# Optimization experiments

Measured on AMD Instinct MI355X. Metric: run time of the kernel, lower is better.

Reference implementation:

```python
import jax, jax.numpy as jnp
import numpy as np
from math import log2

B, N, H, DH, BSZ = 4, 4096, 16, 64, 16
DIM = H * DH
EPS = 1e-8


def setup_inputs() -> dict:
    key = jax.random.key(0)
    ks = jax.random.split(key, 7)
    s = 0.02
    return {
        "hidden_states": jax.random.normal(ks[0], (B, N, DIM), jnp.float32),
        "Wq": jax.random.normal(ks[1], (DIM, DIM), jnp.float32) * s,
        "bq": jax.random.normal(ks[2], (DIM,), jnp.float32) * s,
        "Wk": jax.random.normal(ks[3], (DIM, DIM), jnp.float32) * s,
        "bk": jax.random.normal(ks[4], (DIM,), jnp.float32) * s,
        "Wv": jax.random.normal(ks[5], (DIM, DIM), jnp.float32) * s,
        "bv": jax.random.normal(ks[6], (DIM,), jnp.float32) * s,
    }


def _hattention(q, k, v):
    # q, k, v: [(b*h), n, dh]; n is a power of two divisible by BSZ
    bh, n, dh = q.shape
    num_levels = int(log2(n // BSZ)) - 2  # coarsen until 4 blocks remain

    # coarsening: mean-pool q and k, sum-pool v (mask=None path)
    qkvs = [(q, k, v)]
    for _ in range(num_levels):
        q = q.reshape(bh, -1, 2, dh).mean(axis=2)
        k = k.reshape(bh, -1, 2, dh).mean(axis=2)
        v = v.reshape(bh, -1, 2, dh).sum(axis=2)
        qkvs.append((q, k, v))

    def flip_blocks(t):
        # swap adjacent blocks to capture off-diagonal interactions
        nb = t.shape[1]
        return t.reshape(bh, nb // 2, 2, BSZ, dh)[:, :, ::-1].reshape(bh, nb, BSZ, dh)

    Ys = []
    L = len(qkvs)
    for ind in range(L):
        qq, kk, vv = qkvs[L - 1 - ind]  # reversed: coarsest first
        is_last = ind == L - 1          # finest level: pure block-diagonal
        blk = lambda t: t.reshape(bh, -1, BSZ, dh)
        qq, kk, vv = blk(qq), blk(kk), blk(vv)
        if not is_last:
            kk = flip_blocks(kk)
            vv = flip_blocks(vv)
        S = jnp.einsum('bnid,bnjd->bnij', qq, kk)
        S = S - jnp.max(S, axis=-1, keepdims=True)
        A = jnp.exp(S)  # unnormalized attention weights
        y = jnp.einsum('bnij,bnjd->bnid', A, vv)
        Ys.append((y.reshape(bh, -1, dh), A.sum(axis=-1).reshape(bh, -1)))

    # interpolate: upsample coarse numerators/denominators and accumulate
    Y, A = Ys[0]
    for Y_l, A_l in Ys[1:]:
        Y = jnp.repeat(Y, 2, axis=1) + Y_l
        A = jnp.repeat(A, 2, axis=1) + A_l
    return Y / (A + EPS)[..., None]


def reference(hidden_states, Wq, bq, Wk, bk, Wv, bv):
    b, n, d = hidden_states.shape
    q = hidden_states @ Wq + bq
    k = hidden_states @ Wk + bk
    v = hidden_states @ Wv + bv
    split_heads = lambda t: t.reshape(b, n, H, DH).transpose(0, 2, 1, 3).reshape(b * H, n, DH)
    q, k, v = split_heads(q), split_heads(k), split_heads(v)
    q = q * (DH ** -0.5)
    out = _hattention(q, k, v)  # [(b*h), n, dh]
    return out.reshape(b, H, n, DH).transpose(0, 2, 1, 3).reshape(b, n, H * DH)
```

## Files before the change

### kernel.cpp

```cpp
#include <hip/hip_runtime.h>
#include <hip/hip_bf16.h>

typedef unsigned short u16;
typedef unsigned int u32;
typedef __bf16 bf16x8 __attribute__((ext_vector_type(8)));
typedef float f32x4 __attribute__((ext_vector_type(4)));
typedef u16 u16x4 __attribute__((ext_vector_type(4)));
typedef u16 u16x8 __attribute__((ext_vector_type(8)));

#define N_    4096
#define H_    16
#define BH_   64
#define DIM_  1024
#define MTOK  16384

#define RB1 262144
#define RB2 393216
#define RB3 458752
#define RB4 491520
#define RB5 507904
#define RB6 516096

__device__ __forceinline__ float bf2f(u16 u) {
  union { u32 i; float f; } x; x.i = ((u32)u) << 16; return x.f;
}
__device__ __forceinline__ u16 f2bf(float f) {
  union { float f; u32 i; } x; x.f = f;
  u32 r = x.i + 0x7fffu + ((x.i >> 16) & 1u);
  return (u16)(r >> 16);
}

__device__ __forceinline__ void gload_lds16(const u16* g, u16* l) {
  __builtin_amdgcn_global_load_lds(
      (const __attribute__((address_space(1))) void*)g,
      (__attribute__((address_space(3))) void*)l, 16, 0, 0);
}

__global__ __launch_bounds__(256) void k_prep(const float* __restrict__ hid,
                                              u16* __restrict__ hidb,
                                              const float* __restrict__ Wq,
                                              const float* __restrict__ Wk,
                                              const float* __restrict__ Wv,
                                              u16* __restrict__ Wt) {
  __shared__ float tile[32][33];
  const int bx = blockIdx.x;
  if (bx < 16384) {
    int i = bx * 256 + threadIdx.x;
    f32x4 v = reinterpret_cast<const f32x4*>(hid)[i];
    u16x4 o;
    o[0] = f2bf(v[0]); o[1] = f2bf(v[1]); o[2] = f2bf(v[2]); o[3] = f2bf(v[3]);
    reinterpret_cast<u16x4*>(hidb)[i] = o;
  } else {
    const int bid = bx - 16384;
    const int zz = bid >> 10;
    const int rem = bid & 1023;
    const int n0 = (rem & 31) * 32, k0 = (rem >> 5) * 32;
    const float* W = (zz == 0) ? Wq : ((zz == 1) ? Wk : Wv);
    const int tx = threadIdx.x & 31, ty = threadIdx.x >> 5;
    #pragma unroll
    for (int r = ty; r < 32; r += 8)
      tile[r][tx] = W[(size_t)(k0 + r) * DIM_ + n0 + tx];
    __syncthreads();
    u16* o = Wt + (size_t)zz * DIM_ * DIM_;
    #pragma unroll
    for (int r = ty; r < 32; r += 8)
      o[(size_t)(n0 + r) * DIM_ + k0 + tx] = f2bf(tile[tx][r]);
  }
}

__global__ __launch_bounds__(256, 2) void k_qkv_gemm(
    const u16* __restrict__ hid,
    const u16* __restrict__ Wt,
    const float* __restrict__ bq, const float* __restrict__ bk, const float* __restrict__ bv,
    u16* __restrict__ qout, u16* __restrict__ kout, u16* __restrict__ vout) {
  const int m0 = blockIdx.x * 128;
  const int n0 = blockIdx.y * 128;
  __shared__ u16 As[128 * 64];
  __shared__ u16 Bs[3][128 * 64];
  const int t = threadIdx.x;
  const int lane = t & 63, wave = t >> 6;
  const int wm = (wave >> 1) * 64, wn = (wave & 1) * 64;
  f32x4 acc[3][4][4];
  #pragma unroll
  for (int z = 0; z < 3; z++)
    #pragma unroll
    for (int m = 0; m < 4; m++)
      #pragma unroll
      for (int n = 0; n < 4; n++) acc[z][m][n] = (f32x4){0.f, 0.f, 0.f, 0.f};

  const int srow = t >> 3;
  const int sslot = (t & 7) ^ (srow & 7);
  const u16* Ag = hid + ((size_t)m0 + srow) * DIM_ + sslot * 8;
  const u16* Bg = Wt + ((size_t)n0 + srow) * DIM_ + sslot * 8;
  u16* AsT = &As[t * 8];
  const int lr = lane & 15, kg = lane >> 4;

  for (int k0 = 0; k0 < DIM_; k0 += 64) {
    #pragma unroll
    for (int j = 0; j < 4; j++)
      gload_lds16(Ag + k0 + j * (32 * DIM_), AsT + j * 2048);
    #pragma unroll
    for (int z = 0; z < 3; z++)
      #pragma unroll
      for (int j = 0; j < 4; j++)
        gload_lds16(Bg + (size_t)z * DIM_ * DIM_ + k0 + j * (32 * DIM_),
                    &Bs[z][t * 8 + j * 2048]);
    __syncthreads();
    #pragma unroll
    for (int ks = 0; ks < 2; ks++) {
      const int sw = ((ks * 4 + kg) ^ (lr & 7)) * 8;
      bf16x8 af[4];
      #pragma unroll
      for (int m = 0; m < 4; m++)
        af[m] = *reinterpret_cast<const bf16x8*>(&As[(wm + m * 16 + lr) * 64 + sw]);
      #pragma unroll
      for (int z = 0; z < 3; z++) {
        bf16x8 bfr[4];
        #pragma unroll
        for (int n = 0; n < 4; n++)
          bfr[n] = *reinterpret_cast<const bf16x8*>(&Bs[z][(wn + n * 16 + lr) * 64 + sw]);
        __builtin_amdgcn_s_setprio(1);
        #pragma unroll
        for (int m = 0; m < 4; m++)
          #pragma unroll
          for (int n = 0; n < 4; n++)
            acc[z][m][n] =
                __builtin_amdgcn_mfma_f32_16x16x32_bf16(af[m], bfr[n], acc[z][m][n], 0, 0, 0);
        __builtin_amdgcn_s_setprio(0);
      }
    }
    __syncthreads();
  }

  const int rg = lane >> 4;
  const int b = m0 >> 12;
  const int posb = m0 & (N_ - 1);
  const int h = (n0 + wn) >> 6;
  const size_t bh = (size_t)(b * H_ + h);

  #pragma unroll
  for (int z = 0; z < 3; z++) {
    const float* bias = (z == 0) ? bq : ((z == 1) ? bk : bv);
    u16* dst = (z == 0) ? qout : ((z == 1) ? kout : vout);
    const float scale = (z == 0) ? 0.125f : 1.0f;
    const bool isv = (z == 2);
    const float s1 = isv ? 1.f : 0.5f, s2 = isv ? 1.f : 0.25f;
    const float s3 = isv ? 1.f : 0.125f, s4 = isv ? 1.f : 0.0625f;
    const float s5 = isv ? 1.f : 0.03125f, s6 = isv ? 1.f : 0.015625f;
    float c5a[4], c5b[4];
    #pragma unroll
    for (int n = 0; n < 4; n++) { c5a[n] = 0.f; c5b[n] = 0.f; }
    #pragma unroll
    for (int m = 0; m < 4; m++) {
      const int plm = wm + m * 16;
      #pragma unroll
      for (int n = 0; n < 4; n++) {
        const int d = n * 16 + lr;
        const float bias_v = bias[n0 + wn + d];
        float v0 = (acc[z][m][n][0] + bias_v) * scale;
        float v1 = (acc[z][m][n][1] + bias_v) * scale;
        float v2 = (acc[z][m][n][2] + bias_v) * scale;
        float v3 = (acc[z][m][n][3] + bias_v) * scale;
        const int pl = plm + rg * 4;
        size_t r0 = (bh * N_ + posb + pl) * 64 + d;
        dst[r0] = f2bf(v0); dst[r0 + 64] = f2bf(v1);
        dst[r0 + 128] = f2bf(v2); dst[r0 + 192] = f2bf(v3);
        float c1a = v0 + v1, c1b = v2 + v3;
        size_t r1 = ((size_t)RB1 + bh * 2048 + (size_t)((posb + pl) >> 1)) * 64 + d;
        dst[r1] = f2bf(c1a * s1);
        dst[r1 + 64] = f2bf(c1b * s1);
        float c2 = c1a + c1b;
        dst[((size_t)RB2 + bh * 1024 + (size_t)((posb + pl) >> 2)) * 64 + d] = f2bf(c2 * s2);
        float c3 = c2 + __shfl_xor(c2, 16);
        float c4 = c3 + __shfl_xor(c3, 32);
        if ((rg & 1) == 0)
          dst[((size_t)RB3 + bh * 512 + (size_t)(((posb + plm) >> 3) + (rg >> 1))) * 64 + d] =
              f2bf(c3 * s3);
        if (rg == 0)
          dst[((size_t)RB4 + bh * 256 + (size_t)((posb + plm) >> 4)) * 64 + d] = f2bf(c4 * s4);
        if (m < 2) c5a[n] += c4; else c5b[n] += c4;
      }
    }
    if (rg == 0) {
      const int r5 = (posb + wm) >> 5;
      const int r6 = (posb + wm) >> 6;
      #pragma unroll
      for (int n = 0; n < 4; n++) {
        const int d = n * 16 + lr;
        dst[((size_t)RB5 + bh * 128 + (size_t)r5) * 64 + d] = f2bf(c5a[n] * s5);
        dst[((size_t)RB5 + bh * 128 + (size_t)(r5 + 1)) * 64 + d] = f2bf(c5b[n] * s5);
        dst[((size_t)RB6 + bh * 64 + (size_t)r6) * 64 + d] = f2bf((c5a[n] + c5b[n]) * s6);
      }
    }
  }
}

__device__ __forceinline__ void qk_softmax(const u16* __restrict__ qb_, size_t qrow,
                                           const u16* __restrict__ kb_, size_t kvrow,
                                           int lane, f32x4& p, float& asum) {
  const int lr = lane & 15, g = lane >> 4;
  const u16* kp = kb_ + (kvrow + lr) * 64 + g * 8;
  const u16* qp = qb_ + (qrow + lr) * 64 + g * 8;
  bf16x8 ka0 = *reinterpret_cast<const bf16x8*>(kp);
  bf16x8 ka1 = *reinterpret_cast<const bf16x8*>(kp + 32);
  bf16x8 qa0 = *reinterpret_cast<const bf16x8*>(qp);
  bf16x8 qa1 = *reinterpret_cast<const bf16x8*>(qp + 32);
  f32x4 s = (f32x4){0.f, 0.f, 0.f, 0.f};
  s = __builtin_amdgcn_mfma_f32_16x16x32_bf16(ka0, qa0, s, 0, 0, 0);
  s = __builtin_amdgcn_mfma_f32_16x16x32_bf16(ka1, qa1, s, 0, 0, 0);
  float mx = fmaxf(fmaxf(s[0], s[1]), fmaxf(s[2], s[3]));
  mx = fmaxf(mx, __shfl_xor(mx, 16));
  mx = fmaxf(mx, __shfl_xor(mx, 32));
  #pragma unroll
  for (int i = 0; i < 4; i++) p[i] = __expf(s[i] - mx);
  asum = p[0] + p[1] + p[2] + p[3];
  asum += __shfl_xor(asum, 16);
  asum += __shfl_xor(asum, 32);
}

__device__ __forceinline__ bf16x8 prep_pb(const f32x4& p, int lane) {
  const int g = lane >> 4;
  const int src = (lane & 15) + ((g & 1) << 5);
  float tl[4], th[4];
  #pragma unroll
  for (int i = 0; i < 4; i++) {
    tl[i] = __shfl(p[i], src);
    th[i] = __shfl(p[i], src + 16);
  }
  const bool act = (g < 2);
  union { u16 u[8]; bf16x8 b; } cvt;
  #pragma unroll
  for (int i = 0; i < 4; i++) {
    cvt.u[i] = act ? f2bf(tl[i]) : (u16)0;
    cvt.u[4 + i] = act ? f2bf(th[i]) : (u16)0;
  }
  return cvt.b;
}

__device__ __forceinline__ f32x4 pv_chunk(const u16* __restrict__ vb_, size_t kvrow,
                                          int c, int lane, bf16x8 pb) {
  const int lr = lane & 15, g = lane >> 4;
  const u16* vp = vb_ + (kvrow + (size_t)(g & 1) * 8) * 64 + c * 16 + lr;
  union { u16 u[8]; bf16x8 b; } va;
  #pragma unroll
  for (int e = 0; e < 8; e++) va.u[e] = vp[(size_t)e * 64];
  f32x4 y = (f32x4){0.f, 0.f, 0.f, 0.f};
  return __builtin_amdgcn_mfma_f32_16x16x32_bf16(va.b, pb, y, 0, 0, 0);
}

__global__ __launch_bounds__(256) void k_attn_rest(
    const u16* __restrict__ qb, const u16* __restrict__ kb, const u16* __restrict__ vb,
    u16* __restrict__ Yb, float* __restrict__ Ab) {
  const int wid = blockIdx.x * 4 + (threadIdx.x >> 6);
  const int lane = threadIdx.x & 63;
  const int rb = wid * 16;
  int r = rb, lnl = 11;
  while (r >= (64 << lnl)) { r -= (64 << lnl); --lnl; }
  const int posl = r & ((1 << lnl) - 1);
  const size_t qrow = (size_t)RB1 + rb;
  const size_t kvrow = qrow - posl + ((size_t)((((posl >> 4) ^ 1)) & ((1 << (lnl - 4)) - 1)) << 4);

  f32x4 p; float asum;
  qk_softmax(qb, qrow, kb, kvrow, lane, p, asum);
  if (lane < 16) Ab[rb + lane] = asum;
  bf16x8 pb = prep_pb(p, lane);

  const int lr = lane & 15, g = lane >> 4;
  #pragma unroll
  for (int c = 0; c < 4; c++) {
    f32x4 y = pv_chunk(vb, kvrow, c, lane, pb);
    u16x4 o;
    #pragma unroll
    for (int i = 0; i < 4; i++) o[i] = f2bf(y[i]);
    *reinterpret_cast<u16x4*>(Yb + (size_t)(rb + lr) * 64 + c * 16 + g * 4) = o;
  }
}

__global__ __launch_bounds__(256) void k_attn0(
    const u16* __restrict__ qb, const u16* __restrict__ kb, const u16* __restrict__ vb,
    const u16* __restrict__ Yb, const float* __restrict__ Ab, float* __restrict__ out) {
  const int wid = blockIdx.x * 4 + (threadIdx.x >> 6);
  const int lane = threadIdx.x & 63;
  const int rb = wid * 16;
  const int bh = rb >> 12, posb = rb & 4095;
  const size_t qrow = (size_t)rb, kvrow = (size_t)rb;

  f32x4 p; float asum;
  qk_softmax(qb, qrow, kb, kvrow, lane, p, asum);
  bf16x8 pb = prep_pb(p, lane);

  const int lr = lane & 15, g = lane >> 4;
  const int pos = posb + lr;
  float den = asum + 1e-8f;
  int ybase[6];
  #pragma unroll
  for (int l = 1; l <= 6; l++) {
    int st = 262144 - (262144 >> (l - 1));
    int idx = st + (bh << (12 - l)) + (pos >> l);
    den += Ab[idx];
    ybase[l - 1] = idx;
  }
  const float inv = 1.0f / den;

  const int b = bh >> 4, h = bh & 15;
  float* op = out + ((size_t)(b * N_ + pos)) * DIM_ + h * 64;
  #pragma unroll
  for (int c = 0; c < 4; c++) {
    f32x4 y = pv_chunk(vb, kvrow, c, lane, pb);
    #pragma unroll
    for (int l = 0; l < 6; l++) {
      u16x4 cy = *reinterpret_cast<const u16x4*>(Yb + (size_t)ybase[l] * 64 + c * 16 + g * 4);
      #pragma unroll
      for (int i = 0; i < 4; i++) y[i] += bf2f(cy[i]);
    }
    f32x4 w;
    #pragma unroll
    for (int i = 0; i < 4; i++) w[i] = y[i] * inv;
    *reinterpret_cast<f32x4*>(op + c * 16 + g * 4) = w;
  }
}

extern "C" void kernel_launch(void* const* d_in, const int* in_sizes, int n_in,
                              void* d_out, int out_size, void* d_ws, size_t ws_size,
                              hipStream_t stream) {
  const float* hid = (const float*)d_in[0];
  const float* Wq = (const float*)d_in[1];
  const float* bq = (const float*)d_in[2];
  const float* Wk = (const float*)d_in[3];
  const float* bk = (const float*)d_in[4];
  const float* Wv = (const float*)d_in[5];
  const float* bv = (const float*)d_in[6];
  float* out = (float*)d_out;
  char* ws = (char*)d_ws;

  u16* hidb = (u16*)(ws + 0);
  u16* Wt   = (u16*)(ws + 33554432);
  u16* Yb   = (u16*)(ws + 0);
  float* Ab = (float*)(ws + 33030144);
  u16* qb   = (u16*)(ws + 39845888);
  u16* kb   = (u16*)(ws + 106430464);
  u16* vb   = (u16*)(ws + 173015040);

  k_prep<<<19456, 256, 0, stream>>>(hid, hidb, Wq, Wk, Wv, Wt);
  k_qkv_gemm<<<dim3(128, 8, 1), 256, 0, stream>>>(hidb, Wt, bq, bk, bv, qb, kb, vb);
  k_attn_rest<<<4032, 256, 0, stream>>>(qb, kb, vb, Yb, Ab);
  k_attn0<<<4096, 256, 0, stream>>>(qb, kb, vb, Yb, Ab, out);
}
```

Baseline: 212.1 us.

## Double-buffer QKV GEMM shared tiles and split work across eight waves

The fused QKV GEMM now uses 512 threads (8 waves, each computing a 32x64 sub-tile) and double-buffers the A/B shared-memory tiles, so the global-to-LDS loads for the next K step are issued before the MFMAs of the current step. Each wave holds half the accumulators, which cuts register pressure. The level-6 pooled sums now span two waves and are combined through an LDS scratch area after a barrier. Shared memory doubles to 128 KB per block, which lowers how many blocks fit on a CU and makes the launch_bounds(512,2) request unlikely to be met.

```diff
diff --git a/kernel.cpp b/kernel.cpp
--- a/kernel.cpp
+++ b/kernel.cpp
@@ -68,75 +68,82 @@
   }
 }
 
-__global__ __launch_bounds__(256, 2) void k_qkv_gemm(
+__global__ __launch_bounds__(512, 2) void k_qkv_gemm(
     const u16* __restrict__ hid,
     const u16* __restrict__ Wt,
     const float* __restrict__ bq, const float* __restrict__ bk, const float* __restrict__ bv,
     u16* __restrict__ qout, u16* __restrict__ kout, u16* __restrict__ vout) {
   const int m0 = blockIdx.x * 128;
   const int n0 = blockIdx.y * 128;
-  __shared__ u16 As[128 * 64];
-  __shared__ u16 Bs[3][128 * 64];
+  __shared__ u16 As[2][8192];
+  __shared__ u16 Bs[2][3][8192];
   const int t = threadIdx.x;
   const int lane = t & 63, wave = t >> 6;
-  const int wm = (wave >> 1) * 64, wn = (wave & 1) * 64;
-  f32x4 acc[3][4][4];
+  const int wm4 = wave >> 1, wn2 = wave & 1;
+  f32x4 acc[3][2][4];
   #pragma unroll
   for (int z = 0; z < 3; z++)
     #pragma unroll
-    for (int m = 0; m < 4; m++)
-      #pragma unroll
-      for (int n = 0; n < 4; n++) acc[z][m][n] = (f32x4){0.f, 0.f, 0.f, 0.f};
+    for (int mf = 0; mf < 2; mf++)
+      #pragma unroll
+      for (int nf = 0; nf < 4; nf++) acc[z][mf][nf] = (f32x4){0.f, 0.f, 0.f, 0.f};
 
   const int srow = t >> 3;
   const int sslot = (t & 7) ^ (srow & 7);
   const u16* Ag = hid + ((size_t)m0 + srow) * DIM_ + sslot * 8;
   const u16* Bg = Wt + ((size_t)n0 + srow) * DIM_ + sslot * 8;
-  u16* AsT = &As[t * 8];
   const int lr = lane & 15, kg = lane >> 4;
 
-  for (int k0 = 0; k0 < DIM_; k0 += 64) {
-    #pragma unroll
-    for (int j = 0; j < 4; j++)
-      gload_lds16(Ag + k0 + j * (32 * DIM_), AsT + j * 2048);
+  auto stage = [&](int d, int k0) {
+    #pragma unroll
+    for (int j = 0; j < 2; j++)
+      gload_lds16(Ag + k0 + j * (64 * DIM_), &As[d][j * 4096 + t * 8]);
     #pragma unroll
     for (int z = 0; z < 3; z++)
       #pragma unroll
-      for (int j = 0; j < 4; j++)
-        gload_lds16(Bg + (size_t)z * DIM_ * DIM_ + k0 + j * (32 * DIM_),
-                    &Bs[z][t * 8 + j * 2048]);
-    __syncthreads();
+      for (int j = 0; j < 2; j++)
+        gload_lds16(Bg + (size_t)z * DIM_ * DIM_ + k0 + j * (64 * DIM_),
+                    &Bs[d][z][j * 4096 + t * 8]);
+  };
+
+  stage(0, 0);
+  __syncthreads();
+  for (int tau = 0; tau < 16; ++tau) {
+    const int cur = tau & 1;
+    if (tau < 15) stage(cur ^ 1, (tau + 1) * 64);
     #pragma unroll
     for (int ks = 0; ks < 2; ks++) {
       const int sw = ((ks * 4 + kg) ^ (lr & 7)) * 8;
-      bf16x8 af[4];
-      #pragma unroll
-      for (int m = 0; m < 4; m++)
-        af[m] = *reinterpret_cast<const bf16x8*>(&As[(wm + m * 16 + lr) * 64 + sw]);
+      bf16x8 af[2];
+      #pragma unroll
+      for (int mf = 0; mf < 2; mf++)
+        af[mf] = *reinterpret_cast<const bf16x8*>(&As[cur][(wm4 * 32 + mf * 16 + lr) * 64 + sw]);
       #pragma unroll
       for (int z = 0; z < 3; z++) {
         bf16x8 bfr[4];
         #pragma unroll
-        for (int n = 0; n < 4; n++)
-          bfr[n] = *reinterpret_cast<const bf16x8*>(&Bs[z][(wn + n * 16 + lr) * 64 + sw]);
+        for (int nf = 0; nf < 4; nf++)
+          bfr[nf] =
+              *reinterpret_cast<const bf16x8*>(&Bs[cur][z][(wn2 * 64 + nf * 16 + lr) * 64 + sw]);
         __builtin_amdgcn_s_setprio(1);
         #pragma unroll
-        for (int m = 0; m < 4; m++)
+        for (int mf = 0; mf < 2; mf++)
           #pragma unroll
-          for (int n = 0; n < 4; n++)
-            acc[z][m][n] =
-                __builtin_amdgcn_mfma_f32_16x16x32_bf16(af[m], bfr[n], acc[z][m][n], 0, 0, 0);
+          for (int nf = 0; nf < 4; nf++)
+            acc[z][mf][nf] =
+                __builtin_amdgcn_mfma_f32_16x16x32_bf16(af[mf], bfr[nf], acc[z][mf][nf], 0, 0, 0);
         __builtin_amdgcn_s_setprio(0);
       }
     }
     __syncthreads();
   }
 
-  const int rg = lane >> 4;
+  const int rg = kg;
   const int b = m0 >> 12;
   const int posb = m0 & (N_ - 1);
-  const int h = (n0 + wn) >> 6;
+  const int h = (n0 >> 6) + wn2;
   const size_t bh = (size_t)(b * H_ + h);
+  float* scr = (float*)&As[0][0];
 
   #pragma unroll
   for (int z = 0; z < 3; z++) {
@@ -146,21 +153,21 @@
     const bool isv = (z == 2);
     const float s1 = isv ? 1.f : 0.5f, s2 = isv ? 1.f : 0.25f;
     const float s3 = isv ? 1.f : 0.125f, s4 = isv ? 1.f : 0.0625f;
-    const float s5 = isv ? 1.f : 0.03125f, s6 = isv ? 1.f : 0.015625f;
-    float c5a[4], c5b[4];
-    #pragma unroll
-    for (int n = 0; n < 4; n++) { c5a[n] = 0.f; c5b[n] = 0.f; }
-    #pragma unroll
-    for (int m = 0; m < 4; m++) {
-      const int plm = wm + m * 16;
-      #pragma unroll
-      for (int n = 0; n < 4; n++) {
-        const int d = n * 16 + lr;
-        const float bias_v = bias[n0 + wn + d];
-        float v0 = (acc[z][m][n][0] + bias_v) * scale;
-        float v1 = (acc[z][m][n][1] + bias_v) * scale;
-        float v2 = (acc[z][m][n][2] + bias_v) * scale;
-        float v3 = (acc[z][m][n][3] + bias_v) * scale;
+    const float s5 = isv ? 1.f : 0.03125f;
+    float c5[4];
+    #pragma unroll
+    for (int nf = 0; nf < 4; nf++) c5[nf] = 0.f;
+    #pragma unroll
+    for (int mf = 0; mf < 2; mf++) {
+      const int plm = wm4 * 32 + mf * 16;
+      #pragma unroll
+      for (int nf = 0; nf < 4; nf++) {
+        const int d = nf * 16 + lr;
+        const float bias_v = bias[n0 + wn2 * 64 + d];
+        float v0 = (acc[z][mf][nf][0] + bias_v) * scale;
+        float v1 = (acc[z][mf][nf][1] + bias_v) * scale;
+        float v2 = (acc[z][mf][nf][2] + bias_v) * scale;
+        float v3 = (acc[z][mf][nf][3] + bias_v) * scale;
         const int pl = plm + rg * 4;
         size_t r0 = (bh * N_ + posb + pl) * 64 + d;
         dst[r0] = f2bf(v0); dst[r0 + 64] = f2bf(v1);
@@ -178,18 +185,32 @@
               f2bf(c3 * s3);
         if (rg == 0)
           dst[((size_t)RB4 + bh * 256 + (size_t)((posb + plm) >> 4)) * 64 + d] = f2bf(c4 * s4);
-        if (m < 2) c5a[n] += c4; else c5b[n] += c4;
+        c5[nf] += c4;
       }
     }
     if (rg == 0) {
-      const int r5 = (posb + wm) >> 5;
-      const int r6 = (posb + wm) >> 6;
-      #pragma unroll
-      for (int n = 0; n < 4; n++) {
-        const int d = n * 16 + lr;
-        dst[((size_t)RB5 + bh * 128 + (size_t)r5) * 64 + d] = f2bf(c5a[n] * s5);
-        dst[((size_t)RB5 + bh * 128 + (size_t)(r5 + 1)) * 64 + d] = f2bf(c5b[n] * s5);
-        dst[((size_t)RB6 + bh * 64 + (size_t)r6) * 64 + d] = f2bf((c5a[n] + c5b[n]) * s6);
+      const int r5 = (posb + wm4 * 32) >> 5;
+      #pragma unroll
+      for (int nf = 0; nf < 4; nf++) {
+        const int d = nf * 16 + lr;
+        dst[((size_t)RB5 + bh * 128 + (size_t)r5) * 64 + d] = f2bf(c5[nf] * s5);
+        scr[((wave * 3 + z) * 4 + nf) * 16 + lr] = c5[nf];
+      }
+    }
+  }
+  __syncthreads();
+  if ((wm4 & 1) == 0 && rg == 0) {
+    const int r6 = (posb + wm4 * 32) >> 6;
+    #pragma unroll
+    for (int z = 0; z < 3; z++) {
+      u16* dst = (z == 0) ? qout : ((z == 1) ? kout : vout);
+      const float s6 = (z == 2) ? 1.f : 0.015625f;
+      #pragma unroll
+      for (int nf = 0; nf < 4; nf++) {
+        const int d = nf * 16 + lr;
+        float own = scr[((wave * 3 + z) * 4 + nf) * 16 + lr];
+        float par = scr[(((wave + 2) * 3 + z) * 4 + nf) * 16 + lr];
+        dst[((size_t)RB6 + bh * 64 + (size_t)r6) * 64 + d] = f2bf((own + par) * s6);
       }
     }
   }
@@ -342,7 +363,7 @@
   u16* vb   = (u16*)(ws + 173015040);
 
   k_prep<<<19456, 256, 0, stream>>>(hid, hidb, Wq, Wk, Wv, Wt);
-  k_qkv_gemm<<<dim3(128, 8, 1), 256, 0, stream>>>(hidb, Wt, bq, bk, bv, qb, kb, vb);
+  k_qkv_gemm<<<dim3(128, 8), 512, 0, stream>>>(hidb, Wt, bq, bk, bv, qb, kb, vb);
   k_attn_rest<<<4032, 256, 0, stream>>>(qb, kb, vb, Yb, Ab);
   k_attn0<<<4096, 256, 0, stream>>>(qb, kb, vb, Yb, Ab, out);
 }
```

Result: slower. 247.7 us (+16.8%).
